# Performance work log

Hardware: AMD Instinct MI355X
Metric: run time of the kernel (lower is better)

## Reference

```python
import jax, jax.numpy as jnp
import numpy as np


def conv3x3(x, w, b):
    # x: [B,1,H,W], w: [1,1,3,3] (OIHW), b: [1]; stride 1, padding 1
    y = jax.lax.conv_general_dilated(x, w, (1, 1), 'SAME',
                                     dimension_numbers=('NCHW', 'OIHW', 'NCHW'))
    return y + b[0]


def avg_pool(x, k):
    B, C, H, W = x.shape
    return x.reshape(B, C, H // k, k, W // k, k).mean(axis=(3, 5))


def nearest_up(x, k):
    # nearest-neighbor upsample by integer factor k (matches torch 'nearest')
    return jnp.repeat(jnp.repeat(x, k, axis=2), k, axis=3)


def conv1x1(x, w):
    # x: [B,3,H,W], w: [1,3,1,1] -> [B,1,H,W]
    return jnp.einsum('bchw,oc->bohw', x, w[:, :, 0, 0])


def setup_inputs() -> dict:
    key = jax.random.key(0)
    ks = jax.random.split(key, 16)
    B, H, W = 8, 512, 512
    std = 0.005
    inp = {
        'x':          jax.random.normal(ks[0], (B, 1, H, W), jnp.float32),
        'downSample': jax.random.normal(ks[1], (B, 1, H // 2, W // 2), jnp.float32),
        'upSample':   jax.random.normal(ks[2], (B, 1, 2 * H, 2 * W), jnp.float32),
        'BU':         jax.random.normal(ks[3], (B, 1, H, W), jnp.float32),
        'BUdown':     jax.random.normal(ks[4], (B, 1, H // 2, W // 2), jnp.float32),
        'BUup':       jax.random.normal(ks[5], (B, 1, 2 * H, 2 * W), jnp.float32),
        'convAx': std * jax.random.normal(ks[6], (1, 1, 3, 3), jnp.float32),
        'biasx':  std * jax.random.normal(ks[7], (1,), jnp.float32),
        'convAd': std * jax.random.normal(ks[8], (1, 1, 3, 3), jnp.float32),
        'biasd':  std * jax.random.normal(ks[9], (1,), jnp.float32),
        'convAu': std * jax.random.normal(ks[10], (1, 1, 3, 3), jnp.float32),
        'biasu':  std * jax.random.normal(ks[11], (1,), jnp.float32),
        'conv1x1_x': std * jax.random.normal(ks[12], (1, 3, 1, 1), jnp.float32),
        'conv1x1_d': std * jax.random.normal(ks[13], (1, 3, 1, 1), jnp.float32),
        'conv1x1_u': std * jax.random.normal(ks[14], (1, 3, 1, 1), jnp.float32),
    }
    return inp


def reference(x, downSample, upSample, BU, BUdown, BUup,
              convAx, biasx, convAd, biasd, convAu, biasu,
              conv1x1_x, conv1x1_d, conv1x1_u):
    # 5 iterations of conv3x3 + residual add + clamp(-1,1) per pyramid level
    for _ in range(5):
        x = jnp.clip(conv3x3(x, convAx, biasx) + BU, -1.0, 1.0)
        downSample = jnp.clip(conv3x3(downSample, convAd, biasd) + BUdown, -1.0, 1.0)
        upSample = jnp.clip(conv3x3(upSample, convAu, biasu) + BUup, -1.0, 1.0)
    # cross-scale fusion: resample all three levels to each level and concat
    newx = jnp.concatenate([avg_pool(upSample, 2), x, nearest_up(downSample, 2)], axis=1)
    newUp = jnp.concatenate([upSample, nearest_up(x, 2), nearest_up(downSample, 4)], axis=1)
    newDown = jnp.concatenate([avg_pool(upSample, 4), avg_pool(x, 2), downSample], axis=1)
    x_out = conv1x1(newx, conv1x1_x)
    down_out = conv1x1(newDown, conv1x1_d)
    up_out = conv1x1(newUp, conv1x1_u)
    return (x_out, down_out, up_out)
```

## Files before the change

kernel.cpp:

```cpp
#include <hip/hip_runtime.h>

#define NBATCH 8
#define TW 64
#define TH 32
#define SROWS 42
#define SQUADS 20
#define STRDQ 80
#define NSTRIP 180
#define NTHR 192

__device__ __forceinline__ int lofs(int R, int q) {
    int rot = (3 * (R >> 1)) % 20;
    int p = q + rot;
    if (p >= 20) p -= 20;
    return R * STRDQ + (p << 2);
}

__device__ __forceinline__ void acc_row(float4& v, float L, float4 m, float R,
                                        float ka, float kb, float kc) {
    v.x += ka * L   + kb * m.x + kc * m.y;
    v.y += ka * m.x + kb * m.y + kc * m.z;
    v.z += ka * m.y + kb * m.z + kc * m.w;
    v.w += ka * m.z + kb * m.w + kc * R;
}

__device__ __forceinline__ void clamp_mask(float4& v, float4 pm) {
    v.x = __builtin_amdgcn_fmed3f(v.x, -1.0f, 1.0f) * pm.x;
    v.y = __builtin_amdgcn_fmed3f(v.y, -1.0f, 1.0f) * pm.y;
    v.z = __builtin_amdgcn_fmed3f(v.z, -1.0f, 1.0f) * pm.z;
    v.w = __builtin_amdgcn_fmed3f(v.w, -1.0f, 1.0f) * pm.w;
}

__global__ __launch_bounds__(NTHR, 4) void conv5_all(
    const float* __restrict__ srcU, const float* __restrict__ buU,
    const float* __restrict__ wtU, const float* __restrict__ bsU,
    const float* __restrict__ srcX, const float* __restrict__ buX,
    const float* __restrict__ wtX, const float* __restrict__ bsX,
    const float* __restrict__ srcD, const float* __restrict__ buD,
    const float* __restrict__ wtD, const float* __restrict__ bsD,
    float* __restrict__ dstU, float* __restrict__ dstX, float* __restrict__ dstD)
{
    __shared__ __align__(16) float bufA[SROWS * STRDQ];
    __shared__ __align__(16) float bufB[SROWS * STRDQ];

    const int tid = threadIdx.x;
    const int blk = blockIdx.x;

    const float* src; const float* BU; const float* wt; const float* bs;
    float* dst; int HW; int tx, ty, b;
    if (blk < 4096) {
        src = srcU; BU = buU; wt = wtU; bs = bsU; dst = dstU; HW = 1024;
        b = blk >> 9; int rem = blk & 511; ty = rem >> 4; tx = rem & 15;
    } else if (blk < 5120) {
        int t = blk - 4096;
        src = srcX; BU = buX; wt = wtX; bs = bsX; dst = dstX; HW = 512;
        b = t >> 7; int rem = t & 127; ty = rem >> 3; tx = rem & 7;
    } else {
        int t = blk - 5120;
        src = srcD; BU = buD; wt = wtD; bs = bsD; dst = dstD; HW = 256;
        b = t >> 5; int rem = t & 31; ty = rem >> 2; tx = rem & 3;
    }
    const int bh0 = ty * TH, bw0 = tx * TW;
    const long base = (long)b * HW * HW;

    for (int s = tid; s < SROWS * SQUADS; s += NTHR) {
        int r = s / SQUADS, cq = s - r * SQUADS;
        int gh = bh0 + r - 5;
        int gw = bw0 + (cq << 2) - 8;
        float4 v = {0.0f, 0.0f, 0.0f, 0.0f};
        if ((unsigned)gh < (unsigned)HW) {
            const float* gp = src + base + (long)gh * HW + gw;
            if (gw >= 0 && gw + 3 < HW) {
                v = *(const float4*)gp;
            } else {
                if ((unsigned)(gw + 0) < (unsigned)HW) v.x = gp[0];
                if ((unsigned)(gw + 1) < (unsigned)HW) v.y = gp[1];
                if ((unsigned)(gw + 2) < (unsigned)HW) v.z = gp[2];
                if ((unsigned)(gw + 3) < (unsigned)HW) v.w = gp[3];
            }
        }
        *(float4*)&bufA[lofs(r, cq)] = v;
    }
    for (int s = tid; s < 120; s += NTHR) {
        int r, q;
        if (s < 40)      { r = (s < 20) ? 0 : 41; q = s % 20; }
        else             { int s2 = s - 40; r = 1 + (s2 >> 1); q = (s2 & 1) ? 19 : 0; }
        float4 z = {0.0f, 0.0f, 0.0f, 0.0f};
        *(float4*)&bufB[lofs(r, q)] = z;
    }

    const float k00 = wt[0], k01 = wt[1], k02 = wt[2];
    const float k10 = wt[3], k11 = wt[4], k12 = wt[5];
    const float k20 = wt[6], k21 = wt[7], k22 = wt[8];
    const float bias = bs[0];

    const bool act = (tid < NSTRIP);
    int rp = 0, j = 0;
    {
        int g = (0x75426310u >> ((tid & 7) << 2)) & 0xF;
        int need = tid >> 3;
        for (int r_ = (g & 1); r_ < 20; r_ += 2) {
            int j0 = ((g - 3 * r_) & 7) >> 1;
            int c = (j0 == 0) ? 3 : 2;
            if (need < c) { rp = r_; j = j0 + 4 * need; break; }
            need -= c;
        }
    }

    int rdo[4][4];
    #pragma unroll
    for (int r = 0; r < 4; ++r)
        #pragma unroll
        for (int c = 0; c < 4; ++c)
            rdo[r][c] = lofs(2 * rp + r, 2 * j + c);
    int wro[2][2];
    #pragma unroll
    for (int i = 0; i < 2; ++i) {
        wro[i][0] = lofs(2 * rp + 1 + i, 2 * j + 1);
        wro[i][1] = lofs(2 * rp + 1 + i, 2 * j + 2);
    }

    float4 pm0[2], pm1[2];
    float hf[2];
    #pragma unroll
    for (int i = 0; i < 2; ++i) {
        int gh = bh0 + 2 * rp - 4 + i;
        hf[i] = (act && (unsigned)gh < (unsigned)HW) ? 1.0f : 0.0f;
        float* p0 = (float*)&pm0[i]; float* p1 = (float*)&pm1[i];
        #pragma unroll
        for (int k = 0; k < 4; ++k) {
            p0[k] = hf[i] * (((unsigned)(bw0 + 8 * j - 4 + k) < (unsigned)HW) ? 1.0f : 0.0f);
            p1[k] = hf[i] * (((unsigned)(bw0 + 8 * j + k)     < (unsigned)HW) ? 1.0f : 0.0f);
        }
    }
    float4 bu0[2], bu1[2];
    #pragma unroll
    for (int i = 0; i < 2; ++i) {
        int gh = bh0 + 2 * rp - 4 + i;
        bool hok = (hf[i] != 0.0f);
        int gw0 = bw0 + 8 * j - 4;
        const float* bp = BU + base + (long)gh * HW + gw0;
        if (hok && gw0 >= 0 && gw0 + 7 < HW) {
            float4 a = *(const float4*)bp;
            float4 c = *(const float4*)(bp + 4);
            bu0[i] = {a.x + bias, a.y + bias, a.z + bias, a.w + bias};
            bu1[i] = {c.x + bias, c.y + bias, c.z + bias, c.w + bias};
        } else {
            float* b0 = (float*)&bu0[i]; float* b1 = (float*)&bu1[i];
            #pragma unroll
            for (int k = 0; k < 4; ++k) {
                int w0 = gw0 + k;
                int w1 = gw0 + 4 + k;
                b0[k] = (hok && (unsigned)w0 < (unsigned)HW) ? (bp[k] + bias)     : 0.0f;
                b1[k] = (hok && (unsigned)w1 < (unsigned)HW) ? (bp[k + 4] + bias) : 0.0f;
            }
        }
    }

    float* cur = bufA;
    float* nxt = bufB;

    for (int it = 0; it < 5; ++it) {
        __syncthreads();
        if (act) {
            float4 q[4][4];
            #pragma unroll
            for (int r = 0; r < 4; ++r)
                #pragma unroll
                for (int c = 0; c < 4; ++c)
                    q[r][c] = *(const float4*)(cur + rdo[r][c]);
            #pragma unroll
            for (int i = 0; i < 2; ++i) {
                float4 v0 = bu0[i];
                float4 v1 = bu1[i];
                acc_row(v0, q[i][0].w,     q[i][1],     q[i][2].x,     k00, k01, k02);
                acc_row(v0, q[i + 1][0].w, q[i + 1][1], q[i + 1][2].x, k10, k11, k12);
                acc_row(v0, q[i + 2][0].w, q[i + 2][1], q[i + 2][2].x, k20, k21, k22);
                acc_row(v1, q[i][1].w,     q[i][2],     q[i][3].x,     k00, k01, k02);
                acc_row(v1, q[i + 1][1].w, q[i + 1][2], q[i + 1][3].x, k10, k11, k12);
                acc_row(v1, q[i + 2][1].w, q[i + 2][2], q[i + 2][3].x, k20, k21, k22);
                clamp_mask(v0, pm0[i]);
                clamp_mask(v1, pm1[i]);
                *(float4*)(nxt + wro[i][0]) = v0;
                *(float4*)(nxt + wro[i][1]) = v1;
            }
        }
        float* t = cur; cur = nxt; nxt = t;
    }
    __syncthreads();

    for (int i2 = tid; i2 < TH * (TW / 4); i2 += NTHR) {
        int r = i2 >> 4;
        int cq = i2 & 15;
        float4 v = *(const float4*)&cur[lofs(r + 5, cq + 2)];
        *(float4*)&dst[base + (long)(bh0 + r) * HW + bw0 + (cq << 2)] = v;
    }
}

__global__ __launch_bounds__(256) void fuse_all(
    const float* __restrict__ X,
    const float* __restrict__ D,
    const float* __restrict__ U,
    const float* __restrict__ cx,
    const float* __restrict__ cd,
    const float* __restrict__ cu,
    float* __restrict__ xo, float* __restrict__ dno, float* __restrict__ upo)
{
    const int total = NBATCH << 16;
    int idx = blockIdx.x * blockDim.x + threadIdx.x;
    if (idx >= total) return;
    int wd = idx & 255;
    int hd = (idx >> 8) & 255;
    int b  = idx >> 16;

    const float cx0 = cx[0], cx1 = cx[1], cx2 = cx[2];
    const float cd0 = cd[0], cd1 = cd[1], cd2 = cd[2];
    const float cu0 = cu[0], cu1 = cu[1], cu2 = cu[2];

    int ub = (b << 20) + ((hd << 2) << 10) + (wd << 2);
    float4 u0 = *(const float4*)&U[ub];
    float4 u1 = *(const float4*)&U[ub + 1024];
    float4 u2 = *(const float4*)&U[ub + 2048];
    float4 u3 = *(const float4*)&U[ub + 3072];
    int xb = (b << 18) + ((hd << 1) << 9) + (wd << 1);
    float2 x0 = *(const float2*)&X[xb];
    float2 x1 = *(const float2*)&X[xb + 512];
    float dv = D[idx];

    float p00 = 0.25f * (u0.x + u0.y + u1.x + u1.y);
    float p01 = 0.25f * (u0.z + u0.w + u1.z + u1.w);
    float p10 = 0.25f * (u2.x + u2.y + u3.x + u3.y);
    float p11 = 0.25f * (u2.z + u2.w + u3.z + u3.w);
    float pu4 = 0.25f * (p00 + p01 + p10 + p11);
    float px2 = 0.25f * (x0.x + x0.y + x1.x + x1.y);

    dno[idx] = cd0 * pu4 + cd1 * px2 + cd2 * dv;

    float2 xo0, xo1;
    xo0.x = cx0 * p00 + cx1 * x0.x + cx2 * dv;
    xo0.y = cx0 * p01 + cx1 * x0.y + cx2 * dv;
    xo1.x = cx0 * p10 + cx1 * x1.x + cx2 * dv;
    xo1.y = cx0 * p11 + cx1 * x1.y + cx2 * dv;
    *(float2*)&xo[xb]       = xo0;
    *(float2*)&xo[xb + 512] = xo1;

    float4 o0, o1, o2, o3;
    o0.x = cu0 * u0.x + cu1 * x0.x + cu2 * dv;
    o0.y = cu0 * u0.y + cu1 * x0.x + cu2 * dv;
    o0.z = cu0 * u0.z + cu1 * x0.y + cu2 * dv;
    o0.w = cu0 * u0.w + cu1 * x0.y + cu2 * dv;
    o1.x = cu0 * u1.x + cu1 * x0.x + cu2 * dv;
    o1.y = cu0 * u1.y + cu1 * x0.x + cu2 * dv;
    o1.z = cu0 * u1.z + cu1 * x0.y + cu2 * dv;
    o1.w = cu0 * u1.w + cu1 * x0.y + cu2 * dv;
    o2.x = cu0 * u2.x + cu1 * x1.x + cu2 * dv;
    o2.y = cu0 * u2.y + cu1 * x1.x + cu2 * dv;
    o2.z = cu0 * u2.z + cu1 * x1.y + cu2 * dv;
    o2.w = cu0 * u2.w + cu1 * x1.y + cu2 * dv;
    o3.x = cu0 * u3.x + cu1 * x1.x + cu2 * dv;
    o3.y = cu0 * u3.y + cu1 * x1.x + cu2 * dv;
    o3.z = cu0 * u3.z + cu1 * x1.y + cu2 * dv;
    o3.w = cu0 * u3.w + cu1 * x1.y + cu2 * dv;
    *(float4*)&upo[ub]        = o0;
    *(float4*)&upo[ub + 1024] = o1;
    *(float4*)&upo[ub + 2048] = o2;
    *(float4*)&upo[ub + 3072] = o3;
}

extern "C" void kernel_launch(void* const* d_in, const int* in_sizes, int n_in,
                              void* d_out, int out_size, void* d_ws, size_t ws_size,
                              hipStream_t stream)
{
    const float* x    = (const float*)d_in[0];
    const float* down = (const float*)d_in[1];
    const float* up   = (const float*)d_in[2];
    const float* BUx  = (const float*)d_in[3];
    const float* BUd  = (const float*)d_in[4];
    const float* BUu  = (const float*)d_in[5];
    const float* wAx  = (const float*)d_in[6];
    const float* bx   = (const float*)d_in[7];
    const float* wAd  = (const float*)d_in[8];
    const float* bd   = (const float*)d_in[9];
    const float* wAu  = (const float*)d_in[10];
    const float* bu   = (const float*)d_in[11];
    const float* c1x  = (const float*)d_in[12];
    const float* c1d  = (const float*)d_in[13];
    const float* c1u  = (const float*)d_in[14];

    float* out = (float*)d_out;
    float* ws  = (float*)d_ws;

    const int NX = NBATCH * 512 * 512;
    const int ND = NBATCH * 256 * 256;

    float* wsX = ws;
    float* wsD = ws + NX;
    float* wsU = ws + NX + ND;
    float* outX = out;
    float* outD = out + NX;
    float* outU = out + NX + ND;

    conv5_all<<<5376, NTHR, 0, stream>>>(
        up,   BUu, wAu, bu,
        x,    BUx, wAx, bx,
        down, BUd, wAd, bd,
        wsU, wsX, wsD);

    fuse_all<<<(ND + 255) / 256, 256, 0, stream>>>(wsX, wsD, wsU, c1x, c1d, c1u,
                                                   outX, outD, outU);
}
```

Before: 208.4 us.

## Shrink conv tile height, trim LDS reads to scalars, unroll ping-pong iterations

```diff
diff --git a/kernel.cpp b/kernel.cpp
--- a/kernel.cpp
+++ b/kernel.cpp
@@ -2,11 +2,12 @@
 
 #define NBATCH 8
 #define TW 64
-#define TH 32
-#define SROWS 42
+#define TH 26
+#define SROWS 36
 #define SQUADS 20
 #define STRDQ 80
-#define NSTRIP 180
+#define NPAIRS 17
+#define NSTRIP 153
 #define NTHR 192
 
 __device__ __forceinline__ int lofs(int R, int q) {
@@ -48,17 +49,17 @@
 
     const float* src; const float* BU; const float* wt; const float* bs;
     float* dst; int HW; int tx, ty, b;
-    if (blk < 4096) {
+    if (blk < 5120) {
         src = srcU; BU = buU; wt = wtU; bs = bsU; dst = dstU; HW = 1024;
-        b = blk >> 9; int rem = blk & 511; ty = rem >> 4; tx = rem & 15;
-    } else if (blk < 5120) {
-        int t = blk - 4096;
+        b = blk / 640; int rem = blk - b * 640; ty = rem >> 4; tx = rem & 15;
+    } else if (blk < 6400) {
+        int t = blk - 5120;
         src = srcX; BU = buX; wt = wtX; bs = bsX; dst = dstX; HW = 512;
-        b = t >> 7; int rem = t & 127; ty = rem >> 3; tx = rem & 7;
+        b = t / 160; int rem = t - b * 160; ty = rem >> 3; tx = rem & 7;
     } else {
-        int t = blk - 5120;
+        int t = blk - 6400;
         src = srcD; BU = buD; wt = wtD; bs = bsD; dst = dstD; HW = 256;
-        b = t >> 5; int rem = t & 31; ty = rem >> 2; tx = rem & 3;
+        b = t / 40; int rem = t - b * 40; ty = rem >> 2; tx = rem & 3;
     }
     const int bh0 = ty * TH, bw0 = tx * TW;
     const long base = (long)b * HW * HW;
@@ -81,9 +82,9 @@
         }
         *(float4*)&bufA[lofs(r, cq)] = v;
     }
-    for (int s = tid; s < 120; s += NTHR) {
+    for (int s = tid; s < 108; s += NTHR) {
         int r, q;
-        if (s < 40)      { r = (s < 20) ? 0 : 41; q = s % 20; }
+        if (s < 40)      { r = (s < 20) ? 0 : 35; q = s % 20; }
         else             { int s2 = s - 40; r = 1 + (s2 >> 1); q = (s2 & 1) ? 19 : 0; }
         float4 z = {0.0f, 0.0f, 0.0f, 0.0f};
         *(float4*)&bufB[lofs(r, q)] = z;
@@ -99,7 +100,7 @@
     {
         int g = (0x75426310u >> ((tid & 7) << 2)) & 0xF;
         int need = tid >> 3;
-        for (int r_ = (g & 1); r_ < 20; r_ += 2) {
+        for (int r_ = (g & 1); r_ < NPAIRS; r_ += 2) {
             int j0 = ((g - 3 * r_) & 7) >> 1;
             int c = (j0 == 0) ? 3 : 2;
             if (need < c) { rp = r_; j = j0 + 4 * need; break; }
@@ -107,12 +108,15 @@
         }
     }
 
-    int rdo[4][4];
+    int rdo[4][2];
+    int e0o[4], e3o[4];
     #pragma unroll
-    for (int r = 0; r < 4; ++r)
-        #pragma unroll
-        for (int c = 0; c < 4; ++c)
-            rdo[r][c] = lofs(2 * rp + r, 2 * j + c);
+    for (int r = 0; r < 4; ++r) {
+        rdo[r][0] = lofs(2 * rp + r, 2 * j + 1);
+        rdo[r][1] = lofs(2 * rp + r, 2 * j + 2);
+        e0o[r]    = lofs(2 * rp + r, 2 * j) + 3;
+        e3o[r]    = lofs(2 * rp + r, 2 * j + 3);
+    }
     int wro[2][2];
     #pragma unroll
     for (int i = 0; i < 2; ++i) {
@@ -157,43 +161,50 @@
         }
     }
 
-    float* cur = bufA;
-    float* nxt = bufB;
-
-    for (int it = 0; it < 5; ++it) {
+    auto step = [&](const float* __restrict__ cs, float* __restrict__ ns) {
         __syncthreads();
         if (act) {
-            float4 q[4][4];
+            float4 qm[4][2];
+            float  e0[4], e3[4];
             #pragma unroll
-            for (int r = 0; r < 4; ++r)
-                #pragma unroll
-                for (int c = 0; c < 4; ++c)
-                    q[r][c] = *(const float4*)(cur + rdo[r][c]);
+            for (int r = 0; r < 4; ++r) {
+                qm[r][0] = *(const float4*)(cs + rdo[r][0]);
+                qm[r][1] = *(const float4*)(cs + rdo[r][1]);
+                e0[r] = cs[e0o[r]];
+                e3[r] = cs[e3o[r]];
+            }
             #pragma unroll
             for (int i = 0; i < 2; ++i) {
                 float4 v0 = bu0[i];
                 float4 v1 = bu1[i];
-                acc_row(v0, q[i][0].w,     q[i][1],     q[i][2].x,     k00, k01, k02);
-                acc_row(v0, q[i + 1][0].w, q[i + 1][1], q[i + 1][2].x, k10, k11, k12);
-                acc_row(v0, q[i + 2][0].w, q[i + 2][1], q[i + 2][2].x, k20, k21, k22);
-                acc_row(v1, q[i][1].w,     q[i][2],     q[i][3].x,     k00, k01, k02);
-                acc_row(v1, q[i + 1][1].w, q[i + 1][2], q[i + 1][3].x, k10, k11, k12);
-                acc_row(v1, q[i + 2][1].w, q[i + 2][2], q[i + 2][3].x, k20, k21, k22);
+                acc_row(v0, e0[i],       qm[i][0],     qm[i][1].x,     k00, k01, k02);
+                acc_row(v0, e0[i + 1],   qm[i + 1][0], qm[i + 1][1].x, k10, k11, k12);
+                acc_row(v0, e0[i + 2],   qm[i + 2][0], qm[i + 2][1].x, k20, k21, k22);
+                acc_row(v1, qm[i][0].w,     qm[i][1],     e3[i],       k00, k01, k02);
+                acc_row(v1, qm[i + 1][0].w, qm[i + 1][1], e3[i + 1],   k10, k11, k12);
+                acc_row(v1, qm[i + 2][0].w, qm[i + 2][1], e3[i + 2],   k20, k21, k22);
                 clamp_mask(v0, pm0[i]);
                 clamp_mask(v1, pm1[i]);
-                *(float4*)(nxt + wro[i][0]) = v0;
-                *(float4*)(nxt + wro[i][1]) = v1;
+                *(float4*)(ns + wro[i][0]) = v0;
+                *(float4*)(ns + wro[i][1]) = v1;
             }
         }
-        float* t = cur; cur = nxt; nxt = t;
-    }
+    };
+
+    step(bufA, bufB);
+    step(bufB, bufA);
+    step(bufA, bufB);
+    step(bufB, bufA);
+    step(bufA, bufB);
     __syncthreads();
 
     for (int i2 = tid; i2 < TH * (TW / 4); i2 += NTHR) {
         int r = i2 >> 4;
         int cq = i2 & 15;
-        float4 v = *(const float4*)&cur[lofs(r + 5, cq + 2)];
-        *(float4*)&dst[base + (long)(bh0 + r) * HW + bw0 + (cq << 2)] = v;
+        if (bh0 + r < HW) {
+            float4 v = *(const float4*)&bufB[lofs(r + 5, cq + 2)];
+            *(float4*)&dst[base + (long)(bh0 + r) * HW + bw0 + (cq << 2)] = v;
+        }
     }
 }
 
@@ -300,7 +311,7 @@
     float* outD = out + NX;
     float* outU = out + NX + ND;
 
-    conv5_all<<<5376, NTHR, 0, stream>>>(
+    conv5_all<<<6720, NTHR, 0, stream>>>(
         up,   BUu, wAu, bu,
         x,    BUx, wAx, bx,
         down, BUd, wAd, bd,
```

Result: slower. 215.9 us (+3.6%).

## Enlarge conv tiles to 54 rows and reuse register results across iterations

Applied to the files above, without the earlier changes.

```diff
diff --git a/kernel.cpp b/kernel.cpp
--- a/kernel.cpp
+++ b/kernel.cpp
@@ -2,12 +2,13 @@
 
 #define NBATCH 8
 #define TW 64
-#define TH 32
-#define SROWS 42
+#define TH 54
+#define SROWS 64
 #define SQUADS 20
 #define STRDQ 80
-#define NSTRIP 180
-#define NTHR 192
+#define NPAIRS 31
+#define NSTRIP 279
+#define NTHR 320
 
 __device__ __forceinline__ int lofs(int R, int q) {
     int rot = (3 * (R >> 1)) % 20;
@@ -31,7 +32,7 @@
     v.w = __builtin_amdgcn_fmed3f(v.w, -1.0f, 1.0f) * pm.w;
 }
 
-__global__ __launch_bounds__(NTHR, 4) void conv5_all(
+__global__ __launch_bounds__(NTHR, 5) void conv5_all(
     const float* __restrict__ srcU, const float* __restrict__ buU,
     const float* __restrict__ wtU, const float* __restrict__ bsU,
     const float* __restrict__ srcX, const float* __restrict__ buX,
@@ -48,17 +49,17 @@
 
     const float* src; const float* BU; const float* wt; const float* bs;
     float* dst; int HW; int tx, ty, b;
-    if (blk < 4096) {
+    if (blk < 2432) {
         src = srcU; BU = buU; wt = wtU; bs = bsU; dst = dstU; HW = 1024;
-        b = blk >> 9; int rem = blk & 511; ty = rem >> 4; tx = rem & 15;
-    } else if (blk < 5120) {
-        int t = blk - 4096;
+        b = blk / 304; int rem = blk - b * 304; ty = rem >> 4; tx = rem & 15;
+    } else if (blk < 3072) {
+        int t = blk - 2432;
         src = srcX; BU = buX; wt = wtX; bs = bsX; dst = dstX; HW = 512;
-        b = t >> 7; int rem = t & 127; ty = rem >> 3; tx = rem & 7;
+        b = t / 80; int rem = t - b * 80; ty = rem >> 3; tx = rem & 7;
     } else {
-        int t = blk - 5120;
+        int t = blk - 3072;
         src = srcD; BU = buD; wt = wtD; bs = bsD; dst = dstD; HW = 256;
-        b = t >> 5; int rem = t & 31; ty = rem >> 2; tx = rem & 3;
+        b = t / 20; int rem = t - b * 20; ty = rem >> 2; tx = rem & 3;
     }
     const int bh0 = ty * TH, bw0 = tx * TW;
     const long base = (long)b * HW * HW;
@@ -81,9 +82,9 @@
         }
         *(float4*)&bufA[lofs(r, cq)] = v;
     }
-    for (int s = tid; s < 120; s += NTHR) {
+    for (int s = tid; s < 164; s += NTHR) {
         int r, q;
-        if (s < 40)      { r = (s < 20) ? 0 : 41; q = s % 20; }
+        if (s < 40)      { r = (s < 20) ? 0 : 63; q = s % 20; }
         else             { int s2 = s - 40; r = 1 + (s2 >> 1); q = (s2 & 1) ? 19 : 0; }
         float4 z = {0.0f, 0.0f, 0.0f, 0.0f};
         *(float4*)&bufB[lofs(r, q)] = z;
@@ -94,15 +95,15 @@
     const float k20 = wt[6], k21 = wt[7], k22 = wt[8];
     const float bias = bs[0];
 
-    const bool act = (tid < NSTRIP);
+    bool act = false;
     int rp = 0, j = 0;
     {
         int g = (0x75426310u >> ((tid & 7) << 2)) & 0xF;
         int need = tid >> 3;
-        for (int r_ = (g & 1); r_ < 20; r_ += 2) {
+        for (int r_ = (g & 1); r_ < NPAIRS; r_ += 2) {
             int j0 = ((g - 3 * r_) & 7) >> 1;
             int c = (j0 == 0) ? 3 : 2;
-            if (need < c) { rp = r_; j = j0 + 4 * need; break; }
+            if (need < c) { rp = r_; j = j0 + 4 * need; act = true; break; }
             need -= c;
         }
     }
@@ -157,18 +158,33 @@
         }
     }
 
-    float* cur = bufA;
-    float* nxt = bufB;
-
-    for (int it = 0; it < 5; ++it) {
+    float4 prev0[2], prev1[2];
+
+    auto step = [&](const float* __restrict__ cs, float* __restrict__ ns,
+                    bool first) {
         __syncthreads();
         if (act) {
             float4 q[4][4];
             #pragma unroll
-            for (int r = 0; r < 4; ++r)
-                #pragma unroll
-                for (int c = 0; c < 4; ++c)
-                    q[r][c] = *(const float4*)(cur + rdo[r][c]);
+            for (int r = 0; r < 4; ++r) {
+                q[r][0] = *(const float4*)(cs + rdo[r][0]);
+                q[r][3] = *(const float4*)(cs + rdo[r][3]);
+            }
+            q[0][1] = *(const float4*)(cs + rdo[0][1]);
+            q[0][2] = *(const float4*)(cs + rdo[0][2]);
+            q[3][1] = *(const float4*)(cs + rdo[3][1]);
+            q[3][2] = *(const float4*)(cs + rdo[3][2]);
+            if (first) {
+                q[1][1] = *(const float4*)(cs + rdo[1][1]);
+                q[1][2] = *(const float4*)(cs + rdo[1][2]);
+                q[2][1] = *(const float4*)(cs + rdo[2][1]);
+                q[2][2] = *(const float4*)(cs + rdo[2][2]);
+            } else {
+                q[1][1] = prev0[0];
+                q[1][2] = prev1[0];
+                q[2][1] = prev0[1];
+                q[2][2] = prev1[1];
+            }
             #pragma unroll
             for (int i = 0; i < 2; ++i) {
                 float4 v0 = bu0[i];
@@ -181,19 +197,28 @@
                 acc_row(v1, q[i + 2][1].w, q[i + 2][2], q[i + 2][3].x, k20, k21, k22);
                 clamp_mask(v0, pm0[i]);
                 clamp_mask(v1, pm1[i]);
-                *(float4*)(nxt + wro[i][0]) = v0;
-                *(float4*)(nxt + wro[i][1]) = v1;
-            }
-        }
-        float* t = cur; cur = nxt; nxt = t;
-    }
+                prev0[i] = v0;
+                prev1[i] = v1;
+                *(float4*)(ns + wro[i][0]) = v0;
+                *(float4*)(ns + wro[i][1]) = v1;
+            }
+        }
+    };
+
+    step(bufA, bufB, true);
+    step(bufB, bufA, false);
+    step(bufA, bufB, false);
+    step(bufB, bufA, false);
+    step(bufA, bufB, false);
     __syncthreads();
 
     for (int i2 = tid; i2 < TH * (TW / 4); i2 += NTHR) {
         int r = i2 >> 4;
         int cq = i2 & 15;
-        float4 v = *(const float4*)&cur[lofs(r + 5, cq + 2)];
-        *(float4*)&dst[base + (long)(bh0 + r) * HW + bw0 + (cq << 2)] = v;
+        if (bh0 + r < HW) {
+            float4 v = *(const float4*)&bufB[lofs(r + 5, cq + 2)];
+            *(float4*)&dst[base + (long)(bh0 + r) * HW + bw0 + (cq << 2)] = v;
+        }
     }
 }
 
@@ -300,7 +325,7 @@
     float* outD = out + NX;
     float* outU = out + NX + ND;
 
-    conv5_all<<<5376, NTHR, 0, stream>>>(
+    conv5_all<<<3232, NTHR, 0, stream>>>(
         up,   BUu, wAu, bu,
         x,    BUx, wAx, bx,
         down, BUd, wAd, bd,
```

Measured after the change: 229.3 us. +10.0%, slower.
